# Kernel tuning notes

Hardware: AMD Instinct MI355X
Metric: run time of the kernel (lower is better)

The kernel has to match this reference:

```python
import jax, jax.numpy as jnp
import numpy as np


def _l2norm(v, eps=1e-12):
    # torch F.normalize: v / max(||v||, eps)
    n = jnp.sqrt(jnp.sum(v * v, axis=-1, keepdims=True))
    return v / jnp.maximum(n, eps)


def setup_inputs() -> dict:
    key = jax.random.key(0)
    ks = jax.random.split(key, 5)
    B, D_in, D_out, N = 8192, 1024, 768, 16384
    x = jax.random.normal(ks[0], (B, D_in), dtype=jnp.float32)
    # Linear init ~ U(-1/sqrt(in), 1/sqrt(in)) in torch; scaled randn is fine for a numeric baseline
    W = jax.random.normal(ks[1], (D_out, D_in), dtype=jnp.float32) * (1.0 / np.sqrt(D_in))
    b = jax.random.normal(ks[2], (D_out,), dtype=jnp.float32) * 0.01
    # set_cache() stores L2-normalized keys/values
    cache_keys = _l2norm(jax.random.normal(ks[3], (N, D_out), dtype=jnp.float32))
    cache_values = _l2norm(jax.random.normal(ks[4], (N, D_out), dtype=jnp.float32))
    beta = jnp.asarray(5.0, dtype=jnp.float32)
    alpha = jnp.asarray(1.0, dtype=jnp.float32)
    return {"x": x, "W": W, "b": b, "cache_keys": cache_keys,
            "cache_values": cache_values, "beta": beta, "alpha": alpha}


def reference(x, W, b, cache_keys, cache_values, beta, alpha):
    # Linear projection: [B, D_in] @ [D_in, D_out] + b -> [B, D_out]
    projected = jnp.einsum("bi,oi->bo", x, W) + b
    # L2 normalize queries
    pn = _l2norm(projected)
    # Cosine similarity against cache keys: [B, N]
    similarity = jnp.einsum("bo,no->bn", pn, cache_keys)
    weights = jax.nn.softmax(beta * similarity, axis=-1)
    # Weighted cache read: [B, N] @ [N, D_out] -> [B, D_out]
    retrieved = jnp.einsum("bn,no->bo", weights, cache_values)
    return projected + alpha * retrieved
```

## Files before the change

kernel.cpp:

```cpp
#include <hip/hip_runtime.h>
#include <hip/hip_bf16.h>
#include <hip/hip_fp8.h>

typedef unsigned char  u8;
typedef unsigned short u16;
typedef unsigned int   u32;
typedef __attribute__((ext_vector_type(8)))  short bf16x8;
typedef __attribute__((ext_vector_type(4)))  float f32x4;
typedef __attribute__((ext_vector_type(4)))  int   i32x4;
typedef __attribute__((ext_vector_type(16))) int   i32x16;
typedef __attribute__((ext_vector_type(4)))  u16   u16x4;

__device__ __forceinline__ u16 f2bf(float f) {
  union { float f; u32 u; } v; v.f = f;
  u32 r = v.u + 0x7FFFu + ((v.u >> 16) & 1u);
  return (u16)(r >> 16);
}
__device__ __forceinline__ int q127(float x) { return (int)rintf(x * 127.0f); }

#define GLL16(gptr, lptr)                                                            \
  __builtin_amdgcn_global_load_lds((const __attribute__((address_space(1))) u32*)(gptr), \
                                   (__attribute__((address_space(3))) u32*)(lptr), 16, 0, 0)

#define BARRIER_LGKM() do { asm volatile("s_waitcnt lgkmcnt(0)" ::: "memory"); \
                            __builtin_amdgcn_s_barrier(); } while (0)

__global__ __launch_bounds__(256) void cvt_bf16(const float* __restrict__ in,
                                                u16* __restrict__ out, int n4) {
  int i = blockIdx.x * blockDim.x + threadIdx.x;
  int stride = gridDim.x * blockDim.x;
  for (; i < n4; i += stride) {
    float4 v = ((const float4*)in)[i];
    u16x4 o = { f2bf(v.x), f2bf(v.y), f2bf(v.z), f2bf(v.w) };
    ((u16x4*)out)[i] = o;
  }
}

__global__ __launch_bounds__(256) void buildK(const float* __restrict__ in,
                                              u8* __restrict__ out) {
  __shared__ float tile[64][65];
  int kt = blockIdx.x;
  int t = threadIdx.x;
  int r0 = t >> 6, c = t & 63;
  for (int dc = 0; dc < 12; ++dc) {
    if (dc) __syncthreads();
#pragma unroll
    for (int i = 0; i < 16; ++i) {
      int r = i * 4 + r0;
      tile[r][c] = in[(size_t)(kt * 64 + r) * 768 + dc * 64 + c];
    }
    __syncthreads();
    int d8l = t >> 5, kl = t & 31;
#pragma unroll
    for (int j = 0; j < 2; ++j) {
      int key = j * 32 + kl;
      int s0 = q127(tile[key][d8l * 8 + 0]), s1 = q127(tile[key][d8l * 8 + 1]);
      int s2 = q127(tile[key][d8l * 8 + 2]), s3 = q127(tile[key][d8l * 8 + 3]);
      int s4 = q127(tile[key][d8l * 8 + 4]), s5 = q127(tile[key][d8l * 8 + 5]);
      int s6 = q127(tile[key][d8l * 8 + 6]), s7 = q127(tile[key][d8l * 8 + 7]);
      u32 lo = (s0 & 255) | ((s1 & 255) << 8) | ((s2 & 255) << 16) | ((u32)(s3 & 255) << 24);
      u32 hi = (s4 & 255) | ((s5 & 255) << 8) | ((s6 & 255) << 16) | ((u32)(s7 & 255) << 24);
      uint2 val = { lo, hi };
      *(uint2*)(out + (size_t)(dc * 8 + d8l) * 131072 + (size_t)(kt * 64 + key) * 8) = val;
    }
  }
}

__global__ __launch_bounds__(256) void buildV(const float* __restrict__ in,
                                              u8* __restrict__ out) {
  __shared__ float tile[64][65];
  int kt = blockIdx.x;
  int t = threadIdx.x;
  int r0 = t >> 6, c = t & 63;
  for (int dc = 0; dc < 12; ++dc) {
    if (dc) __syncthreads();
#pragma unroll
    for (int i = 0; i < 16; ++i) {
      int r = i * 4 + r0;
      tile[r][c] = in[(size_t)(kt * 64 + r) * 768 + dc * 64 + c];
    }
    __syncthreads();
    int sub = t >> 5, dl = t & 31;
#pragma unroll
    for (int j = 0; j < 2; ++j) {
      int d = j * 32 + dl;
      int s0 = q127(tile[sub * 8 + 0][d]), s1 = q127(tile[sub * 8 + 1][d]);
      int s2 = q127(tile[sub * 8 + 2][d]), s3 = q127(tile[sub * 8 + 3][d]);
      int s4 = q127(tile[sub * 8 + 4][d]), s5 = q127(tile[sub * 8 + 5][d]);
      int s6 = q127(tile[sub * 8 + 6][d]), s7 = q127(tile[sub * 8 + 7][d]);
      u32 lo = (s0 & 255) | ((s1 & 255) << 8) | ((s2 & 255) << 16) | ((u32)(s3 & 255) << 24);
      u32 hi = (s4 & 255) | ((s5 & 255) << 8) | ((s6 & 255) << 16) | ((u32)(s7 & 255) << 24);
      uint2 val = { lo, hi };
      *(uint2*)(out + (size_t)(kt * 8 + sub) * 6144 + (size_t)(dc * 64 + d) * 8) = val;
    }
  }
}

__global__ __launch_bounds__(256) void gemm1(const u16* __restrict__ A,
                                             const u16* __restrict__ B,
                                             const float* __restrict__ bias,
                                             float* __restrict__ C) {
  __shared__ u16 As[2][128 * 32];
  __shared__ u16 Bs[2][128 * 32];
  int t = threadIdx.x;
  int brow = blockIdx.x * 128, bcol = blockIdx.y * 128;
  int w = t >> 6, l = t & 63;
  int l15 = l & 15, l4 = l >> 4;
  int wr = (w >> 1) * 64, wc = (w & 1) * 64;
  f32x4 acc[4][4];
#pragma unroll
  for (int i = 0; i < 4; ++i)
#pragma unroll
    for (int j = 0; j < 4; ++j) acc[i][j] = f32x4{0.f, 0.f, 0.f, 0.f};

  auto stage = [&](int buf, int kt) {
#pragma unroll
    for (int i = 0; i < 2; ++i) {
      int id = t + i * 256;
      int row = id >> 2, c = id & 3;
      int cs = (c ^ (row & 3)) * 8;
      GLL16(A + (size_t)(brow + row) * 1024 + kt * 32 + cs, &As[buf][id * 8]);
      GLL16(B + (size_t)(bcol + row) * 1024 + kt * 32 + cs, &Bs[buf][id * 8]);
    }
  };
  stage(0, 0);
  for (int kt = 0; kt < 32; ++kt) {
    int buf = kt & 1;
    __syncthreads();
    if (kt < 31) stage(buf ^ 1, kt + 1);
    bf16x8 a[4], b[4];
#pragma unroll
    for (int mf = 0; mf < 4; ++mf) {
      int row = wr + mf * 16 + l15;
      a[mf] = *(const bf16x8*)&As[buf][row * 32 + ((l4 ^ (row & 3)) * 8)];
    }
#pragma unroll
    for (int nf = 0; nf < 4; ++nf) {
      int row = wc + nf * 16 + l15;
      b[nf] = *(const bf16x8*)&Bs[buf][row * 32 + ((l4 ^ (row & 3)) * 8)];
    }
#pragma unroll
    for (int mf = 0; mf < 4; ++mf)
#pragma unroll
      for (int nf = 0; nf < 4; ++nf)
        acc[mf][nf] = __builtin_amdgcn_mfma_f32_16x16x32_bf16(a[mf], b[nf], acc[mf][nf], 0, 0, 0);
  }
#pragma unroll
  for (int mf = 0; mf < 4; ++mf)
#pragma unroll
    for (int nf = 0; nf < 4; ++nf) {
      int col = bcol + wc + nf * 16 + l15;
      float bv = bias[col];
#pragma unroll
      for (int j = 0; j < 4; ++j) {
        int row = brow + wr + mf * 16 + l4 * 4 + j;
        C[(size_t)row * 768 + col] = acc[mf][nf][j] + bv;
      }
    }
}

__global__ __launch_bounds__(384) void rownorm8(const float* __restrict__ P,
                                                u8* __restrict__ q8) {
  int row = blockIdx.x, t = threadIdx.x;
  size_t base = (size_t)row * 768;
  float2 v = *(const float2*)&P[base + 2 * t];
  float ss = v.x * v.x + v.y * v.y;
#pragma unroll
  for (int o = 32; o; o >>= 1) ss += __shfl_xor(ss, o);
  __shared__ float wsum[6];
  if ((t & 63) == 0) wsum[t >> 6] = ss;
  __syncthreads();
  float tot = wsum[0] + wsum[1] + wsum[2] + wsum[3] + wsum[4] + wsum[5];
  float inv = 1.0f / fmaxf(sqrtf(tot), 1e-12f);
  int a = q127(v.x * inv), b = q127(v.y * inv);
  *(u16*)(q8 + base + 2 * t) = (u16)((a & 255) | ((b & 255) << 8));
}

__global__ __launch_bounds__(1024, 4) void attn(const u8* __restrict__ q8,
                                                const u8* __restrict__ Ki8,
                                                const u8* __restrict__ Vi8,
                                                const float* __restrict__ beta_p,
                                                u16* __restrict__ Opart,
                                                float* __restrict__ lpart) {
  __shared__ long Qlds[96 * 64];
  __shared__ long Ps[2][64 * 64];
  __shared__ float lred[16][64];
  int t = threadIdx.x;
  int w = t >> 6, l = t & 63;
  int ql = l & 31, hi = l >> 5;
  int l15 = l & 15, l4g = l >> 4;
  int split = blockIdx.x, qb = blockIdx.y;
  int qrow0 = qb * 64;
  float beta = beta_p[0];
  float c1 = beta * 1.44269504089f / 16129.0f;
  float pscale = 127.0f / expf(beta);
  float ovs = expf(beta) / 16129.0f;

#pragma unroll
  for (int i = 0; i < 6; ++i) {
    int id = i * 1024 + t;
    int c8 = id >> 6, q = id & 63;
    Qlds[c8 * 64 + q] = *(const long*)(q8 + (size_t)(qrow0 + q) * 768 + (size_t)c8 * 8);
  }

  i32x4 oacc[4][3];
#pragma unroll
  for (int mq = 0; mq < 4; ++mq)
#pragma unroll
    for (int nd = 0; nd < 3; ++nd) oacc[mq][nd] = i32x4{0, 0, 0, 0};
  float lsum0 = 0.f, lsum1 = 0.f;

  int kbase = split * 8192;
  const long* Kp = (const long*)Ki8 + (size_t)(2 * hi) * 16384 + (size_t)(kbase + w * 32 + ql);
  const long* Vp = (const long*)Vi8 + ((size_t)(kbase >> 3) + 2 * l4g) * 768 + (size_t)(w * 48 + l15);

  long kb[3][2];
#pragma unroll
  for (int s = 0; s < 3; ++s) {
    kb[s][0] = Kp[(size_t)(4 * s) * 16384];
    kb[s][1] = Kp[(size_t)(4 * s + 1) * 16384];
  }

  __syncthreads();

  for (int it = 0; it < 16; ++it) {
    int n0 = it * 512;
    const long* kp = Kp + n0;
    long* psb = &Ps[it & 1][0];

    i32x16 sacc0 = (i32x16)0;
    i32x16 sacc1 = (i32x16)0;
    __builtin_amdgcn_s_setprio(1);
#pragma unroll
    for (int ks = 0; ks < 24; ++ks) {
      union { long l[2]; i32x4 v; } av, q0u, q1u;
      av.l[0] = kb[ks % 3][0];
      av.l[1] = kb[ks % 3][1];
      if (ks < 21) {
        kb[ks % 3][0] = kp[(size_t)(4 * (ks + 3)) * 16384];
        kb[ks % 3][1] = kp[(size_t)(4 * (ks + 3) + 1) * 16384];
      }
      q0u.l[0] = Qlds[(4 * ks + 2 * hi) * 64 + ql];
      q0u.l[1] = Qlds[(4 * ks + 2 * hi + 1) * 64 + ql];
      q1u.l[0] = Qlds[(4 * ks + 2 * hi) * 64 + ql + 32];
      q1u.l[1] = Qlds[(4 * ks + 2 * hi + 1) * 64 + ql + 32];
      sacc0 = __builtin_amdgcn_mfma_i32_32x32x32_i8(av.v, q0u.v, sacc0, 0, 0, 0);
      sacc1 = __builtin_amdgcn_mfma_i32_32x32x32_i8(av.v, q1u.v, sacc1, 0, 0, 0);
    }
    __builtin_amdgcn_s_setprio(0);

#pragma unroll
    for (int qf = 0; qf < 2; ++qf) {
      int q = ql + qf * 32;
      float lacc = 0.f;
#pragma unroll
      for (int rg = 0; rg < 4; ++rg) {
        float p0, p1, p2, p3;
        if (qf == 0) {
          p0 = exp2f(c1 * (float)sacc0[rg * 4 + 0]); p1 = exp2f(c1 * (float)sacc0[rg * 4 + 1]);
          p2 = exp2f(c1 * (float)sacc0[rg * 4 + 2]); p3 = exp2f(c1 * (float)sacc0[rg * 4 + 3]);
        } else {
          p0 = exp2f(c1 * (float)sacc1[rg * 4 + 0]); p1 = exp2f(c1 * (float)sacc1[rg * 4 + 1]);
          p2 = exp2f(c1 * (float)sacc1[rg * 4 + 2]); p3 = exp2f(c1 * (float)sacc1[rg * 4 + 3]);
        }
        lacc += (p0 + p1) + (p2 + p3);
        int i0 = (int)rintf(fminf(p0 * pscale, 127.f));
        int i1 = (int)rintf(fminf(p1 * pscale, 127.f));
        int i2 = (int)rintf(fminf(p2 * pscale, 127.f));
        int i3 = (int)rintf(fminf(p3 * pscale, 127.f));
        u32 pk = (u32)i0 | ((u32)i1 << 8) | ((u32)i2 << 16) | ((u32)i3 << 24);
        ((u32*)psb)[(w * 4 + rg) * 128 + q * 2 + hi] = pk;
      }
      if (qf == 0) lsum0 += lacc; else lsum1 += lacc;
    }

    if (it < 15) {
      const long* kpn = Kp + (size_t)(it + 1) * 512;
#pragma unroll
      for (int s = 0; s < 3; ++s) {
        kb[s][0] = kpn[(size_t)(4 * s) * 16384];
        kb[s][1] = kpn[(size_t)(4 * s + 1) * 16384];
      }
    }
    long vb[2][3][2];
#pragma unroll
    for (int nd = 0; nd < 3; ++nd) {
      size_t off = (size_t)(n0 >> 3) * 768 + nd * 16;
      vb[0][nd][0] = Vp[off];
      vb[0][nd][1] = Vp[off + 768];
    }

    BARRIER_LGKM();

    __builtin_amdgcn_s_setprio(1);
#pragma unroll
    for (int ksv = 0; ksv < 8; ++ksv) {
      int cur = ksv & 1;
      if (ksv < 7) {
#pragma unroll
        for (int nd = 0; nd < 3; ++nd) {
          size_t off = ((size_t)(n0 >> 3) + (ksv + 1) * 8) * 768 + nd * 16;
          vb[cur ^ 1][nd][0] = Vp[off];
          vb[cur ^ 1][nd][1] = Vp[off + 768];
        }
      }
      union { long l[2]; i32x4 v; } v0, v1, v2;
      v0.l[0] = vb[cur][0][0]; v0.l[1] = vb[cur][0][1];
      v1.l[0] = vb[cur][1][0]; v1.l[1] = vb[cur][1][1];
      v2.l[0] = vb[cur][2][0]; v2.l[1] = vb[cur][2][1];
#pragma unroll
      for (int mq = 0; mq < 4; ++mq) {
        union { long l[2]; i32x4 v; } pa;
        pa.l[0] = psb[(8 * ksv + 2 * l4g) * 64 + mq * 16 + l15];
        pa.l[1] = psb[(8 * ksv + 2 * l4g + 1) * 64 + mq * 16 + l15];
        oacc[mq][0] = __builtin_amdgcn_mfma_i32_16x16x64_i8(pa.v, v0.v, oacc[mq][0], 0, 0, 0);
        oacc[mq][1] = __builtin_amdgcn_mfma_i32_16x16x64_i8(pa.v, v1.v, oacc[mq][1], 0, 0, 0);
        oacc[mq][2] = __builtin_amdgcn_mfma_i32_16x16x64_i8(pa.v, v2.v, oacc[mq][2], 0, 0, 0);
      }
    }
    __builtin_amdgcn_s_setprio(0);
  }

  {
    float s0 = lsum0 + __shfl_xor(lsum0, 32);
    float s1 = lsum1 + __shfl_xor(lsum1, 32);
    if (hi == 0) { lred[w][ql] = s0; lred[w][ql + 32] = s1; }
  }
  __syncthreads();
  if (t < 64) {
    float s = 0.f;
#pragma unroll
    for (int ww = 0; ww < 16; ++ww) s += lred[ww][t];
    lpart[split * 8192 + qrow0 + t] = s;
  }

#pragma unroll
  for (int mq = 0; mq < 4; ++mq)
#pragma unroll
    for (int nd = 0; nd < 3; ++nd) {
      int col = w * 48 + nd * 16 + l15;
#pragma unroll
      for (int j = 0; j < 4; ++j) {
        int row = qrow0 + mq * 16 + l4g * 4 + j;
        Opart[((size_t)split * 8192 + row) * 768 + col] = f2bf((float)oacc[mq][nd][j] * ovs);
      }
    }
}

__global__ __launch_bounds__(192) void combine(float* __restrict__ out,
                                               const u16* __restrict__ Opart,
                                               const float* __restrict__ lpart,
                                               const float* __restrict__ alpha_p) {
  int row = blockIdx.x, t = threadIdx.x;
  float scale = alpha_p[0] / (lpart[row] + lpart[8192 + row]);
  size_t base = (size_t)row * 768 + t * 4;
  u16x4 o0 = *(const u16x4*)&Opart[base];
  u16x4 o1 = *(const u16x4*)&Opart[(size_t)6291456 + base];
  float4 cur = *(float4*)&out[base];
  union { u32 u; float f; } c0, c1, c2, c3, d0_, d1_, d2_, d3_;
  c0.u = (u32)o0[0] << 16; c1.u = (u32)o0[1] << 16; c2.u = (u32)o0[2] << 16; c3.u = (u32)o0[3] << 16;
  d0_.u = (u32)o1[0] << 16; d1_.u = (u32)o1[1] << 16; d2_.u = (u32)o1[2] << 16; d3_.u = (u32)o1[3] << 16;
  cur.x += (c0.f + d0_.f) * scale;
  cur.y += (c1.f + d1_.f) * scale;
  cur.z += (c2.f + d2_.f) * scale;
  cur.w += (c3.f + d3_.f) * scale;
  *(float4*)&out[base] = cur;
}

extern "C" void kernel_launch(void* const* d_in, const int* in_sizes, int n_in,
                              void* d_out, int out_size, void* d_ws, size_t ws_size,
                              hipStream_t stream) {
  const float* x      = (const float*)d_in[0];
  const float* W      = (const float*)d_in[1];
  const float* bias   = (const float*)d_in[2];
  const float* keys   = (const float*)d_in[3];
  const float* values = (const float*)d_in[4];
  const float* beta   = (const float*)d_in[5];
  const float* alpha  = (const float*)d_in[6];
  float* out = (float*)d_out;

  char* ws = (char*)d_ws;
  u16* xb    = (u16*)(ws + 0);
  u16* Wb    = (u16*)(ws + 16777216);
  u8*  Ki8   = (u8*) (ws + 18350080);
  u8*  Vi8   = (u8*) (ws + 30932992);
  u8*  q8    = (u8*) (ws + 43515904);
  u16* Opart = (u16*)(ws + 49807360);
  float* lp  = (float*)(ws + 74973184);

  cvt_bf16<<<2048, 256, 0, stream>>>(x, xb, 8192 * 1024 / 4);
  cvt_bf16<<<768, 256, 0, stream>>>(W, Wb, 768 * 1024 / 4);
  buildK<<<256, 256, 0, stream>>>(keys, Ki8);
  buildV<<<256, 256, 0, stream>>>(values, Vi8);
  gemm1<<<dim3(64, 6), 256, 0, stream>>>(xb, Wb, bias, out);
  rownorm8<<<8192, 384, 0, stream>>>(out, q8);
  attn<<<dim3(2, 128), 1024, 0, stream>>>(q8, Ki8, Vi8, beta, Opart, lp);
  combine<<<8192, 192, 0, stream>>>(out, Opart, lp, alpha);
}
```

Baseline: 324.5 us.

## Repack int8 K/V/Q/P layouts into 16-byte chunks for single dwordx4 loads

Changes the prebuilt int8 K and V caches, the Q tile in LDS and the P buffer from 8-byte interleaved layouts to 16-byte contiguous groups. Each MFMA operand can then be fetched with one 128-bit global or LDS load instead of two 64-bit loads. This halves the load instruction count in the inner loops and makes global accesses wider. The build kernels now write uint4 chunks, and the risk lies in the new index arithmetic and possible LDS bank conflicts with the wider accesses.

```diff
diff --git a/kernel.cpp b/kernel.cpp
--- a/kernel.cpp
+++ b/kernel.cpp
@@ -1,6 +1,5 @@
 #include <hip/hip_runtime.h>
 #include <hip/hip_bf16.h>
-#include <hip/hip_fp8.h>
 
 typedef unsigned char  u8;
 typedef unsigned short u16;
@@ -50,19 +49,18 @@
       tile[r][c] = in[(size_t)(kt * 64 + r) * 768 + dc * 64 + c];
     }
     __syncthreads();
-    int d8l = t >> 5, kl = t & 31;
-#pragma unroll
-    for (int j = 0; j < 2; ++j) {
-      int key = j * 32 + kl;
-      int s0 = q127(tile[key][d8l * 8 + 0]), s1 = q127(tile[key][d8l * 8 + 1]);
-      int s2 = q127(tile[key][d8l * 8 + 2]), s3 = q127(tile[key][d8l * 8 + 3]);
-      int s4 = q127(tile[key][d8l * 8 + 4]), s5 = q127(tile[key][d8l * 8 + 5]);
-      int s6 = q127(tile[key][d8l * 8 + 6]), s7 = q127(tile[key][d8l * 8 + 7]);
-      u32 lo = (s0 & 255) | ((s1 & 255) << 8) | ((s2 & 255) << 16) | ((u32)(s3 & 255) << 24);
-      u32 hi = (s4 & 255) | ((s5 & 255) << 8) | ((s6 & 255) << 16) | ((u32)(s7 & 255) << 24);
-      uint2 val = { lo, hi };
-      *(uint2*)(out + (size_t)(dc * 8 + d8l) * 131072 + (size_t)(kt * 64 + key) * 8) = val;
-    }
+    int d16l = t >> 6, key = t & 63;
+    u32 wd[4];
+#pragma unroll
+    for (int g = 0; g < 4; ++g) {
+      u32 v = 0;
+#pragma unroll
+      for (int j = 0; j < 4; ++j)
+        v |= (u32)(q127(tile[key][d16l * 16 + g * 4 + j]) & 255) << (8 * j);
+      wd[g] = v;
+    }
+    uint4 val = { wd[0], wd[1], wd[2], wd[3] };
+    *(uint4*)(out + ((size_t)(dc * 4 + d16l) * 16384 + (size_t)(kt * 64 + key)) * 16) = val;
   }
 }
 
@@ -80,19 +78,18 @@
       tile[r][c] = in[(size_t)(kt * 64 + r) * 768 + dc * 64 + c];
     }
     __syncthreads();
-    int sub = t >> 5, dl = t & 31;
-#pragma unroll
-    for (int j = 0; j < 2; ++j) {
-      int d = j * 32 + dl;
-      int s0 = q127(tile[sub * 8 + 0][d]), s1 = q127(tile[sub * 8 + 1][d]);
-      int s2 = q127(tile[sub * 8 + 2][d]), s3 = q127(tile[sub * 8 + 3][d]);
-      int s4 = q127(tile[sub * 8 + 4][d]), s5 = q127(tile[sub * 8 + 5][d]);
-      int s6 = q127(tile[sub * 8 + 6][d]), s7 = q127(tile[sub * 8 + 7][d]);
-      u32 lo = (s0 & 255) | ((s1 & 255) << 8) | ((s2 & 255) << 16) | ((u32)(s3 & 255) << 24);
-      u32 hi = (s4 & 255) | ((s5 & 255) << 8) | ((s6 & 255) << 16) | ((u32)(s7 & 255) << 24);
-      uint2 val = { lo, hi };
-      *(uint2*)(out + (size_t)(kt * 8 + sub) * 6144 + (size_t)(dc * 64 + d) * 8) = val;
-    }
+    int k16l = t >> 6, dl = t & 63;
+    u32 wd[4];
+#pragma unroll
+    for (int g = 0; g < 4; ++g) {
+      u32 v = 0;
+#pragma unroll
+      for (int j = 0; j < 4; ++j)
+        v |= (u32)(q127(tile[k16l * 16 + g * 4 + j][dl]) & 255) << (8 * j);
+      wd[g] = v;
+    }
+    uint4 val = { wd[0], wd[1], wd[2], wd[3] };
+    *(uint4*)(out + ((size_t)(kt * 4 + k16l) * 768 + (size_t)(dc * 64 + dl)) * 16) = val;
   }
 }
 
@@ -182,8 +179,8 @@
                                                 const float* __restrict__ beta_p,
                                                 u16* __restrict__ Opart,
                                                 float* __restrict__ lpart) {
-  __shared__ long Qlds[96 * 64];
-  __shared__ long Ps[2][64 * 64];
+  __shared__ i32x4 Qlds[48 * 64];
+  __shared__ i32x4 Ps[2][32 * 64];
   __shared__ float lred[16][64];
   int t = threadIdx.x;
   int w = t >> 6, l = t & 63;
@@ -197,10 +194,10 @@
   float ovs = expf(beta) / 16129.0f;
 
 #pragma unroll
-  for (int i = 0; i < 6; ++i) {
+  for (int i = 0; i < 3; ++i) {
     int id = i * 1024 + t;
-    int c8 = id >> 6, q = id & 63;
-    Qlds[c8 * 64 + q] = *(const long*)(q8 + (size_t)(qrow0 + q) * 768 + (size_t)c8 * 8);
+    int c16 = id >> 6, q = id & 63;
+    Qlds[id] = *(const i32x4*)(q8 + (size_t)(qrow0 + q) * 768 + (size_t)c16 * 16);
   }
 
   i32x4 oacc[4][3];
@@ -211,41 +208,31 @@
   float lsum0 = 0.f, lsum1 = 0.f;
 
   int kbase = split * 8192;
-  const long* Kp = (const long*)Ki8 + (size_t)(2 * hi) * 16384 + (size_t)(kbase + w * 32 + ql);
-  const long* Vp = (const long*)Vi8 + ((size_t)(kbase >> 3) + 2 * l4g) * 768 + (size_t)(w * 48 + l15);
-
-  long kb[3][2];
-#pragma unroll
-  for (int s = 0; s < 3; ++s) {
-    kb[s][0] = Kp[(size_t)(4 * s) * 16384];
-    kb[s][1] = Kp[(size_t)(4 * s + 1) * 16384];
-  }
+  const i32x4* Kp = (const i32x4*)Ki8 + (size_t)hi * 16384 + (size_t)(kbase + w * 32 + ql);
+  const i32x4* Vp = (const i32x4*)Vi8 + ((size_t)(kbase >> 4) + l4g) * 768 + (size_t)(w * 48 + l15);
+
+  i32x4 kb[3];
+#pragma unroll
+  for (int s = 0; s < 3; ++s) kb[s] = Kp[(size_t)(2 * s) * 16384];
 
   __syncthreads();
 
   for (int it = 0; it < 16; ++it) {
     int n0 = it * 512;
-    const long* kp = Kp + n0;
-    long* psb = &Ps[it & 1][0];
+    const i32x4* kp = Kp + n0;
+    i32x4* psb = &Ps[it & 1][0];
 
     i32x16 sacc0 = (i32x16)0;
     i32x16 sacc1 = (i32x16)0;
     __builtin_amdgcn_s_setprio(1);
 #pragma unroll
     for (int ks = 0; ks < 24; ++ks) {
-      union { long l[2]; i32x4 v; } av, q0u, q1u;
-      av.l[0] = kb[ks % 3][0];
-      av.l[1] = kb[ks % 3][1];
-      if (ks < 21) {
-        kb[ks % 3][0] = kp[(size_t)(4 * (ks + 3)) * 16384];
-        kb[ks % 3][1] = kp[(size_t)(4 * (ks + 3) + 1) * 16384];
-      }
-      q0u.l[0] = Qlds[(4 * ks + 2 * hi) * 64 + ql];
-      q0u.l[1] = Qlds[(4 * ks + 2 * hi + 1) * 64 + ql];
-      q1u.l[0] = Qlds[(4 * ks + 2 * hi) * 64 + ql + 32];
-      q1u.l[1] = Qlds[(4 * ks + 2 * hi + 1) * 64 + ql + 32];
-      sacc0 = __builtin_amdgcn_mfma_i32_32x32x32_i8(av.v, q0u.v, sacc0, 0, 0, 0);
-      sacc1 = __builtin_amdgcn_mfma_i32_32x32x32_i8(av.v, q1u.v, sacc1, 0, 0, 0);
+      i32x4 av = kb[ks % 3];
+      if (ks < 21) kb[ks % 3] = kp[(size_t)(2 * (ks + 3)) * 16384];
+      i32x4 q0 = Qlds[(2 * ks + hi) * 64 + ql];
+      i32x4 q1 = Qlds[(2 * ks + hi) * 64 + ql + 32];
+      sacc0 = __builtin_amdgcn_mfma_i32_32x32x32_i8(av, q0, sacc0, 0, 0, 0);
+      sacc1 = __builtin_amdgcn_mfma_i32_32x32x32_i8(av, q1, sacc1, 0, 0, 0);
     }
     __builtin_amdgcn_s_setprio(0);
 
@@ -269,26 +256,20 @@
         int i2 = (int)rintf(fminf(p2 * pscale, 127.f));
         int i3 = (int)rintf(fminf(p3 * pscale, 127.f));
         u32 pk = (u32)i0 | ((u32)i1 << 8) | ((u32)i2 << 16) | ((u32)i3 << 24);
-        ((u32*)psb)[(w * 4 + rg) * 128 + q * 2 + hi] = pk;
+        ((u32*)psb)[((2 * w + (rg >> 1)) * 64 + q) * 4 + 2 * (rg & 1) + hi] = pk;
       }
       if (qf == 0) lsum0 += lacc; else lsum1 += lacc;
     }
 
     if (it < 15) {
-      const long* kpn = Kp + (size_t)(it + 1) * 512;
-#pragma unroll
-      for (int s = 0; s < 3; ++s) {
-        kb[s][0] = kpn[(size_t)(4 * s) * 16384];
-        kb[s][1] = kpn[(size_t)(4 * s + 1) * 16384];
-      }
-    }
-    long vb[2][3][2];
-#pragma unroll
-    for (int nd = 0; nd < 3; ++nd) {
-      size_t off = (size_t)(n0 >> 3) * 768 + nd * 16;
-      vb[0][nd][0] = Vp[off];
-      vb[0][nd][1] = Vp[off + 768];
-    }
+      const i32x4* kpn = Kp + (size_t)(it + 1) * 512;
+#pragma unroll
+      for (int s = 0; s < 3; ++s) kb[s] = kpn[(size_t)(2 * s) * 16384];
+    }
+    i32x4 vb[2][3];
+#pragma unroll
+    for (int nd = 0; nd < 3; ++nd)
+      vb[0][nd] = Vp[(size_t)(n0 >> 4) * 768 + nd * 16];
 
     BARRIER_LGKM();
 
@@ -298,24 +279,15 @@
       int cur = ksv & 1;
       if (ksv < 7) {
 #pragma unroll
-        for (int nd = 0; nd < 3; ++nd) {
-          size_t off = ((size_t)(n0 >> 3) + (ksv + 1) * 8) * 768 + nd * 16;
-          vb[cur ^ 1][nd][0] = Vp[off];
-          vb[cur ^ 1][nd][1] = Vp[off + 768];
-        }
-      }
-      union { long l[2]; i32x4 v; } v0, v1, v2;
-      v0.l[0] = vb[cur][0][0]; v0.l[1] = vb[cur][0][1];
-      v1.l[0] = vb[cur][1][0]; v1.l[1] = vb[cur][1][1];
-      v2.l[0] = vb[cur][2][0]; v2.l[1] = vb[cur][2][1];
+        for (int nd = 0; nd < 3; ++nd)
+          vb[cur ^ 1][nd] = Vp[((size_t)(n0 >> 4) + (ksv + 1) * 4) * 768 + nd * 16];
+      }
 #pragma unroll
       for (int mq = 0; mq < 4; ++mq) {
-        union { long l[2]; i32x4 v; } pa;
-        pa.l[0] = psb[(8 * ksv + 2 * l4g) * 64 + mq * 16 + l15];
-        pa.l[1] = psb[(8 * ksv + 2 * l4g + 1) * 64 + mq * 16 + l15];
-        oacc[mq][0] = __builtin_amdgcn_mfma_i32_16x16x64_i8(pa.v, v0.v, oacc[mq][0], 0, 0, 0);
-        oacc[mq][1] = __builtin_amdgcn_mfma_i32_16x16x64_i8(pa.v, v1.v, oacc[mq][1], 0, 0, 0);
-        oacc[mq][2] = __builtin_amdgcn_mfma_i32_16x16x64_i8(pa.v, v2.v, oacc[mq][2], 0, 0, 0);
+        i32x4 pa = psb[(4 * ksv + l4g) * 64 + mq * 16 + l15];
+        oacc[mq][0] = __builtin_amdgcn_mfma_i32_16x16x64_i8(pa, vb[cur][0], oacc[mq][0], 0, 0, 0);
+        oacc[mq][1] = __builtin_amdgcn_mfma_i32_16x16x64_i8(pa, vb[cur][1], oacc[mq][1], 0, 0, 0);
+        oacc[mq][2] = __builtin_amdgcn_mfma_i32_16x16x64_i8(pa, vb[cur][2], oacc[mq][2], 0, 0, 0);
       }
     }
     __builtin_amdgcn_s_setprio(0);
```

Measured after the change: 284.6 us. 12.3% less time.
